# Kernel tuning notes

Hardware: AMD Instinct MI355X
Metric: run time of the kernel (lower is better)

## Reference

```python
import jax, jax.numpy as jnp
import numpy as np

B, S, D, H = 4, 2048, 1024, 16
DK = D // H

def setup_inputs() -> dict:
    key = jax.random.key(0)
    ks = jax.random.split(key, 5)
    scale = D ** -0.5  # keep activations well-scaled for random weights
    return {
        "x": jax.random.normal(ks[0], (B, S, D), dtype=jnp.float32),
        "w_q": jax.random.normal(ks[1], (D, D), dtype=jnp.float32) * scale,
        "w_k": jax.random.normal(ks[2], (D, D), dtype=jnp.float32) * scale,
        "w_v": jax.random.normal(ks[3], (D, D), dtype=jnp.float32) * scale,
        "w_o": jax.random.normal(ks[4], (D, D), dtype=jnp.float32) * scale,
        "b_o": jnp.zeros((D,), dtype=jnp.float32),
    }

def reference(x, w_q, w_k, w_v, w_o, b_o):
    b, s, d = x.shape
    # nn.Linear applies x @ W^T; project then split heads -> [b, h, s, dk]
    q = (x @ w_q.T).reshape(b, s, H, DK).transpose(0, 2, 1, 3)
    k = (x @ w_k.T).reshape(b, s, H, DK).transpose(0, 2, 1, 3)
    v = (x @ w_v.T).reshape(b, s, H, DK).transpose(0, 2, 1, 3)
    scores = jnp.einsum('bhqd,bhkd->bhqk', q, k) * (DK ** -0.5)
    causal = jnp.tril(jnp.ones((s, s), dtype=bool))  # [s, s]
    scores = jnp.where(causal, scores, jnp.float32(-1e9))
    attn = jax.nn.softmax(scores, axis=-1)
    out = jnp.einsum('bhqk,bhkd->bhqd', attn, v)
    out = out.transpose(0, 2, 1, 3).reshape(b, s, d)
    return out @ w_o.T + b_o
```

## Files before the change

kernel.cpp:

```cpp
#include <hip/hip_runtime.h>

typedef unsigned short u16;
typedef unsigned int u32;
typedef __attribute__((ext_vector_type(4))) u16 u16x4;
typedef __attribute__((ext_vector_type(8))) short short8;
typedef __attribute__((ext_vector_type(4))) float f32x4;
typedef __attribute__((ext_vector_type(16))) float f32x16;
typedef __attribute__((ext_vector_type(4))) u32 uint4v;

#define AS1 __attribute__((address_space(1)))
#define AS3 __attribute__((address_space(3)))

#define B_  4
#define S_  2048
#define D_  1024
#define H_  16
#define DK_ 64

#define WAIT_VM(n) asm volatile("s_waitcnt vmcnt(" #n ")" ::: "memory")
#define WAIT_LGK0  asm volatile("s_waitcnt lgkmcnt(0)" ::: "memory")

__device__ __forceinline__ u16 f2bf(float f) {
  union { float f; unsigned u; } v; v.f = f;
  unsigned r = v.u + 0x7fffu + ((v.u >> 16) & 1u);
  return (u16)(r >> 16);
}

__device__ __forceinline__ u32 cvt_pk_bf16(float lo, float hi) {
  u32 r;
  asm("v_cvt_pk_bf16_f32 %0, %1, %2" : "=v"(r) : "v"(lo), "v"(hi));
  return r;
}

__device__ __forceinline__ void pl32_swap(u32& a, u32& b) {
  asm("v_permlane32_swap_b32 %0, %1" : "+v"(a), "+v"(b));
}

__device__ __forceinline__ void gload_lds16(const void* g, void* l) {
  __builtin_amdgcn_global_load_lds((const AS1 void*)g, (AS3 void*)l, 16, 0, 0);
}

__global__ __launch_bounds__(256) void conv_bf16(const float* __restrict__ in,
                                                 u16* __restrict__ out,
                                                 int n, float scale) {
  int i = (blockIdx.x * 256 + threadIdx.x) * 8;
  if (i >= n) return;
  f32x4 a = *reinterpret_cast<const f32x4*>(in + i);
  f32x4 b = *reinterpret_cast<const f32x4*>(in + i + 4);
  union { u16 u[8]; uint4v v; } r;
#pragma unroll
  for (int j = 0; j < 4; ++j) {
    r.u[j]     = f2bf(a[j] * scale);
    r.u[4 + j] = f2bf(b[j] * scale);
  }
  *reinterpret_cast<uint4v*>(out + i) = r.v;
}

__global__ __launch_bounds__(256) void conv_w4(const float* __restrict__ w0,
                                               const float* __restrict__ w1,
                                               const float* __restrict__ w2,
                                               const float* __restrict__ w3,
                                               u16* __restrict__ out, float s0) {
  int y = blockIdx.y;
  const float* src = (y == 0) ? w0 : (y == 1) ? w1 : (y == 2) ? w2 : w3;
  float scale = (y == 0) ? s0 : 1.0f;
  int i = (blockIdx.x * 256 + threadIdx.x) * 8;
  f32x4 a = *reinterpret_cast<const f32x4*>(src + i);
  f32x4 b = *reinterpret_cast<const f32x4*>(src + i + 4);
  union { u16 u[8]; uint4v v; } r;
#pragma unroll
  for (int j = 0; j < 4; ++j) {
    r.u[j]     = f2bf(a[j] * scale);
    r.u[4 + j] = f2bf(b[j] * scale);
  }
  *reinterpret_cast<uint4v*>(out + (size_t)y * (D_ * D_) + i) = r.v;
}

template<int MODE>
__global__ __launch_bounds__(256) void gemm_bt(const u16* __restrict__ A,
                                               const u16* __restrict__ B,
                                               u16* __restrict__ Qb,
                                               u16* __restrict__ Kb,
                                               u16* __restrict__ Vt,
                                               float* __restrict__ Cf,
                                               const float* __restrict__ bias,
                                               int M, int N, int K) {
  __shared__ __attribute__((aligned(16))) u16 As[128 * 64];
  __shared__ __attribute__((aligned(16))) u16 Bs[128 * 64];

  const int t = threadIdx.x;
  const int l = t & 63;
  const int w = t >> 6;
  const int wr = w >> 1, wc = w & 1;
  const int m0 = blockIdx.y * 128;
  const int n0 = blockIdx.x * 128;

  f32x4 zero = {0.f, 0.f, 0.f, 0.f};
  f32x4 acc[4][4];
#pragma unroll
  for (int i = 0; i < 4; ++i)
#pragma unroll
    for (int j = 0; j < 4; ++j) acc[i][j] = zero;

  for (int k0 = 0; k0 < K; k0 += 64) {
    __syncthreads();
#pragma unroll
    for (int i = 0; i < 4; ++i) {
      int slot = i * 256 + t;
      int r = slot >> 3, c = slot & 7;
      const u16* srcA = A + (size_t)(m0 + r) * K + k0 + ((c ^ (r & 7)) * 8);
      gload_lds16(srcA, (char*)As + (size_t)(i * 256 + w * 64) * 16);
      const u16* srcB = B + (size_t)(n0 + r) * K + k0 + ((c ^ (r & 7)) * 8);
      gload_lds16(srcB, (char*)Bs + (size_t)(i * 256 + w * 64) * 16);
    }
    __syncthreads();

#pragma unroll
    for (int kc = 0; kc < 2; ++kc) {
      short8 a[4], bf[4];
      int lc = kc * 4 + (l >> 4);
#pragma unroll
      for (int i = 0; i < 4; ++i) {
        int ra = wr * 64 + i * 16 + (l & 15);
        a[i] = *reinterpret_cast<const short8*>(&As[ra * 64 + ((lc ^ (ra & 7)) * 8)]);
        int rb = wc * 64 + i * 16 + (l & 15);
        bf[i] = *reinterpret_cast<const short8*>(&Bs[rb * 64 + ((lc ^ (rb & 7)) * 8)]);
      }
#pragma unroll
      for (int mi = 0; mi < 4; ++mi)
#pragma unroll
        for (int ni = 0; ni < 4; ++ni)
          acc[mi][ni] = __builtin_amdgcn_mfma_f32_16x16x32_bf16(a[mi], bf[ni], acc[mi][ni], 0, 0, 0);
    }
  }

#pragma unroll
  for (int ni = 0; ni < 4; ++ni) {
    int col = n0 + wc * 64 + ni * 16 + (l & 15);
    float bv = (MODE == 1) ? bias[col] : 0.f;
#pragma unroll
    for (int mi = 0; mi < 4; ++mi) {
      int row0 = m0 + wr * 64 + mi * 16 + (l >> 4) * 4;
      if (MODE == 1) {
#pragma unroll
        for (int r = 0; r < 4; ++r)
          Cf[(size_t)(row0 + r) * N + col] = acc[mi][ni][r] + bv;
      } else {
        if (col < 2048) {
          u16* dst = (col < 1024) ? Qb : Kb;
          int c = col & 1023;
#pragma unroll
          for (int r = 0; r < 4; ++r)
            dst[(size_t)(row0 + r) * 1024 + c] = f2bf(acc[mi][ni][r]);
        } else {
          int vc = col - 2048;
          int bh = (row0 >> 11) * 16 + (vc >> 6);
          int s0 = row0 & 2047;
          u16x4 pk;
#pragma unroll
          for (int r = 0; r < 4; ++r) pk[r] = f2bf(acc[mi][ni][r]);
          *reinterpret_cast<u16x4*>(Vt + ((size_t)(bh * 64 + (vc & 63))) * 2048 + s0) = pk;
        }
      }
    }
  }
}

__global__ __launch_bounds__(256) void attn_fwd(const u16* __restrict__ Q,
                                                const u16* __restrict__ K,
                                                const u16* __restrict__ Vtg,
                                                u16* __restrict__ AO) {
  __shared__ __attribute__((aligned(16))) u16 smem[24576];
  u16* Ksb = smem;
  u16* Vsb = smem + 12288;

  const int t = threadIdx.x;
  const int l = t & 63;
  const int w = t >> 6;
  const int hi = l >> 5;
  const int hi8 = hi * 8, hi4 = hi * 4;
  const int bh = blockIdx.x;
  const int s = 15 - blockIdx.y;
  const size_t qkbase = (size_t)((bh >> 4) * S_) * D_ + (bh & 15) * DK_;
  const u16* Vg = Vtg + (size_t)bh * 64 * S_;

  const int qw = s * 128 + w * 32;
  const int qi = qw + (l & 31);

  short8 qf[4];
#pragma unroll
  for (int c = 0; c < 4; ++c)
    qf[c] = *reinterpret_cast<const short8*>(Q + qkbase + (size_t)qi * D_ + c * 16 + hi8);

  f32x16 o0 = {0,0,0,0,0,0,0,0,0,0,0,0,0,0,0,0};
  f32x16 o1 = {0,0,0,0,0,0,0,0,0,0,0,0,0,0,0,0};
  float m_r = -INFINITY, l_r = 0.f;

  const int nst = 2 * (s + 1);

  auto stage = [&](int jt, u16* kdst, u16* vdst) {
    const u16* Ksrc = K + qkbase + (size_t)(jt * 64) * D_;
    const u16* Vsrc = Vg + jt * 64;
#pragma unroll
    for (int i = 0; i < 2; ++i) {
      int slot = i * 256 + t;
      int r = slot >> 3, c = t & 7;
      gload_lds16(Ksrc + (size_t)r * D_ + ((c ^ (r & 7)) * 8),
                  (char*)kdst + (size_t)(i * 256 + w * 64) * 16);
      gload_lds16(Vsrc + (size_t)r * S_ + ((c ^ (r & 7)) * 8),
                  (char*)vdst + (size_t)(i * 256 + w * 64) * 16);
    }
  };

  stage(0, Ksb, Vsb);
  stage(1, Ksb + 4096, Vsb + 4096);
  stage(2, Ksb + 8192, Vsb + 8192);
  int o0b = 0, o1b = 4096, o2b = 8192;

  for (int it = 0; it < nst; ++it) {
    if (it < nst - 2)       { WAIT_VM(8); }
    else if (it == nst - 2) { WAIT_VM(4); }
    else                    { WAIT_VM(0); }
    __builtin_amdgcn_s_barrier();
    __builtin_amdgcn_sched_barrier(0);

    const int j0 = it * 64;
    u16* ks = Ksb + o0b;
    u16* vs = Vsb + o0b;

    if (j0 <= qw + 31) {
      f32x16 s0 = {0,0,0,0,0,0,0,0,0,0,0,0,0,0,0,0};
      f32x16 s1 = {0,0,0,0,0,0,0,0,0,0,0,0,0,0,0,0};
#pragma unroll
      for (int c = 0; c < 4; ++c) {
        int cl = 2 * c + hi;
        int k0r = l & 31, k1r = (l & 31) + 32;
        short8 kf0 = *reinterpret_cast<const short8*>(&ks[k0r * 64 + ((cl ^ (k0r & 7)) * 8)]);
        short8 kf1 = *reinterpret_cast<const short8*>(&ks[k1r * 64 + ((cl ^ (k1r & 7)) * 8)]);
        s0 = __builtin_amdgcn_mfma_f32_32x32x16_bf16(kf0, qf[c], s0, 0, 0, 0);
        s1 = __builtin_amdgcn_mfma_f32_32x32x16_bf16(kf1, qf[c], s1, 0, 0, 0);
      }
      if (j0 + 63 > qw) {
#pragma unroll
        for (int r = 0; r < 16; ++r) {
          int key = j0 + (r & 3) + 8 * (r >> 2) + hi4;
          if (key > qi) s0[r] = -INFINITY;
          if (key + 32 > qi) s1[r] = -INFINITY;
        }
      }
      {
        float mx = s0[0];
#pragma unroll
        for (int r = 1; r < 16; ++r) mx = fmaxf(mx, s0[r]);
#pragma unroll
        for (int r = 0; r < 16; ++r) mx = fmaxf(mx, s1[r]);
        mx = fmaxf(mx, __shfl_xor(mx, 32));
        if (!__all(mx <= m_r + 11.0f)) {
          float mnew = fmaxf(m_r, mx);
          float rr = exp2f(m_r - mnew);
          m_r = mnew;
          l_r *= rr;
#pragma unroll
          for (int r = 0; r < 16; ++r) { o0[r] *= rr; o1[r] *= rr; }
        }
        float sum = 0.f;
#pragma unroll
        for (int r = 0; r < 16; ++r) { s0[r] = exp2f(s0[r] - m_r); sum += s0[r]; }
#pragma unroll
        for (int r = 0; r < 16; ++r) { s1[r] = exp2f(s1[r] - m_r); sum += s1[r]; }
        sum += __shfl_xor(sum, 32);
        l_r += sum;
      }
#pragma unroll
      for (int ksl = 0; ksl < 4; ++ksl) {
        const int b = 8 * (ksl & 1);
        const f32x16& ps = (ksl < 2) ? s0 : s1;
        u32 c0 = cvt_pk_bf16(ps[b + 0], ps[b + 1]);
        u32 c1 = cvt_pk_bf16(ps[b + 2], ps[b + 3]);
        u32 c2 = cvt_pk_bf16(ps[b + 4], ps[b + 5]);
        u32 c3 = cvt_pk_bf16(ps[b + 6], ps[b + 7]);
        pl32_swap(c0, c2);
        pl32_swap(c1, c3);
        union { u32 u[4]; short8 s; } pa;
        pa.u[0] = c0; pa.u[1] = c1; pa.u[2] = c2; pa.u[3] = c3;
        int cl = 2 * ksl + hi;
        int d0r = l & 31, d1r = (l & 31) + 32;
        short8 vf0 = *reinterpret_cast<const short8*>(&vs[d0r * 64 + ((cl ^ (d0r & 7)) * 8)]);
        short8 vf1 = *reinterpret_cast<const short8*>(&vs[d1r * 64 + ((cl ^ (d1r & 7)) * 8)]);
        o0 = __builtin_amdgcn_mfma_f32_32x32x16_bf16(vf0, pa.s, o0, 0, 0, 0);
        o1 = __builtin_amdgcn_mfma_f32_32x32x16_bf16(vf1, pa.s, o1, 0, 0, 0);
      }
    }

    WAIT_LGK0;
    __builtin_amdgcn_sched_barrier(0);
    __builtin_amdgcn_s_barrier();
    if (it + 3 < nst) stage(it + 3, Ksb + o0b, Vsb + o0b);
    int tmp = o0b; o0b = o1b; o1b = o2b; o2b = tmp;
  }

  float inv = 1.0f / l_r;
  u16* Ob = smem + w * 2304;
#pragma unroll
  for (int acc = 0; acc < 2; ++acc) {
    const f32x16& oo = acc ? o1 : o0;
#pragma unroll
    for (int rp = 0; rp < 8; ++rp) {
      u32 pk = cvt_pk_bf16(oo[2 * rp] * inv, oo[2 * rp + 1] * inv);
      int d0 = ((2 * rp) & 3) + 8 * (rp >> 1) + hi4 + 32 * acc;
      *reinterpret_cast<u32*>(&Ob[(l & 31) * 72 + d0]) = pk;
    }
  }
  __syncthreads();
  int qq = l >> 1;
  int chb = (l & 1) * 4;
#pragma unroll
  for (int c2 = 0; c2 < 4; ++c2) {
    uint4v vv = *reinterpret_cast<const uint4v*>(&Ob[qq * 72 + (chb + c2) * 8]);
    *reinterpret_cast<uint4v*>(&AO[qkbase + (size_t)(qw - w * 32 + w * 32 + qq) * D_ + (chb + c2) * 8]) = vv;
  }
}

extern "C" void kernel_launch(void* const* d_in, const int* in_sizes, int n_in,
                              void* d_out, int out_size, void* d_ws, size_t ws_size,
                              hipStream_t stream) {
  const float* x  = (const float*)d_in[0];
  const float* wq = (const float*)d_in[1];
  const float* wk = (const float*)d_in[2];
  const float* wv = (const float*)d_in[3];
  const float* wo = (const float*)d_in[4];
  const float* bo = (const float*)d_in[5];
  float* out = (float*)d_out;

  char* ws = (char*)d_ws;
  u16* XB   = (u16*)(ws);
  u16* WQKV = (u16*)(ws + (size_t)(16 << 20));
  u16* WOB  = (u16*)(ws + (size_t)(22 << 20));
  u16* Qb   = (u16*)(ws + (size_t)(24 << 20));
  u16* Kb   = (u16*)(ws + (size_t)(40 << 20));
  u16* Vt   = (u16*)(ws + (size_t)(56 << 20));
  u16* AO   = (u16*)(ws + (size_t)(72 << 20));

  const int nx = B_ * S_ * D_;
  const int nw = D_ * D_;

  conv_bf16<<<nx / 2048, 256, 0, stream>>>(x, XB, nx, 1.0f);
  conv_w4<<<dim3(nw / 2048, 4), 256, 0, stream>>>(wq, wk, wv, wo, WQKV,
                                                  0.18033688011112042f);

  gemm_bt<0><<<dim3(3072 / 128, (B_ * S_) / 128), 256, 0, stream>>>(
      XB, WQKV, Qb, Kb, Vt, nullptr, nullptr, B_ * S_, 3072, D_);

  attn_fwd<<<dim3(B_ * H_, 16), 256, 0, stream>>>(Qb, Kb, Vt, AO);

  gemm_bt<1><<<dim3(D_ / 128, (B_ * S_) / 128), 256, 0, stream>>>(
      AO, WOB, nullptr, nullptr, nullptr, out, bo, B_ * S_, D_, D_);
}
```

Before: 183.0 us.

## Double-buffer GEMM LDS tiles with 512-thread 128x256 blocks and async prefetch

Rewrites the projection GEMM kernel to use 512-thread blocks computing 128x256 tiles, with double-buffered LDS staging so the global-to-LDS loads for tile k+2 run while MFMAs consume tile k. Explicit vmcnt waits, raw barriers, sched_barrier and setprio control the overlap. The goal is to hide global memory latency and reuse A tiles across a wider N. The cost is 96KB of LDS per block, which may limit occupancy, and fewer blocks in the grid for the output projection.

```diff
diff --git a/kernel.cpp b/kernel.cpp
--- a/kernel.cpp
+++ b/kernel.cpp
@@ -77,23 +77,24 @@
 }
 
 template<int MODE>
-__global__ __launch_bounds__(256) void gemm_bt(const u16* __restrict__ A,
-                                               const u16* __restrict__ B,
-                                               u16* __restrict__ Qb,
-                                               u16* __restrict__ Kb,
-                                               u16* __restrict__ Vt,
-                                               float* __restrict__ Cf,
-                                               const float* __restrict__ bias,
-                                               int M, int N, int K) {
-  __shared__ __attribute__((aligned(16))) u16 As[128 * 64];
-  __shared__ __attribute__((aligned(16))) u16 Bs[128 * 64];
+__global__ __launch_bounds__(512, 2) void gemm_bt2(const u16* __restrict__ A,
+                                                   const u16* __restrict__ B,
+                                                   u16* __restrict__ Qb,
+                                                   u16* __restrict__ Kb,
+                                                   u16* __restrict__ Vt,
+                                                   float* __restrict__ Cf,
+                                                   const float* __restrict__ bias,
+                                                   int M, int N, int K) {
+  __shared__ __attribute__((aligned(16))) u16 As[2][128 * 64];
+  __shared__ __attribute__((aligned(16))) u16 Bs[2][256 * 64];
 
   const int t = threadIdx.x;
   const int l = t & 63;
-  const int w = t >> 6;
-  const int wr = w >> 1, wc = w & 1;
+  const int wm = (t >> 6) >> 2;
+  const int wn = (t >> 6) & 3;
   const int m0 = blockIdx.y * 128;
-  const int n0 = blockIdx.x * 128;
+  const int n0 = blockIdx.x * 256;
+  const int NT = K >> 6;
 
   f32x4 zero = {0.f, 0.f, 0.f, 0.f};
   f32x4 acc[4][4];
@@ -102,45 +103,69 @@
 #pragma unroll
     for (int j = 0; j < 4; ++j) acc[i][j] = zero;
 
-  for (int k0 = 0; k0 < K; k0 += 64) {
-    __syncthreads();
+  auto stageA = [&](int kt, int buf) {
+#pragma unroll
+    for (int i = 0; i < 2; ++i) {
+      int slot = i * 512 + t;
+      int r = slot >> 3, c = slot & 7;
+      gload_lds16(A + (size_t)(m0 + r) * K + kt * 64 + ((c ^ (r & 7)) * 8),
+                  (char*)&As[buf][0] + (size_t)slot * 16);
+    }
+  };
+  auto stageB = [&](int kt, int buf) {
 #pragma unroll
     for (int i = 0; i < 4; ++i) {
-      int slot = i * 256 + t;
+      int slot = i * 512 + t;
       int r = slot >> 3, c = slot & 7;
-      const u16* srcA = A + (size_t)(m0 + r) * K + k0 + ((c ^ (r & 7)) * 8);
-      gload_lds16(srcA, (char*)As + (size_t)(i * 256 + w * 64) * 16);
-      const u16* srcB = B + (size_t)(n0 + r) * K + k0 + ((c ^ (r & 7)) * 8);
-      gload_lds16(srcB, (char*)Bs + (size_t)(i * 256 + w * 64) * 16);
-    }
-    __syncthreads();
-
+      gload_lds16(B + (size_t)(n0 + r) * K + kt * 64 + ((c ^ (r & 7)) * 8),
+                  (char*)&Bs[buf][0] + (size_t)slot * 16);
+    }
+  };
+
+  stageA(0, 0); stageB(0, 0);
+  stageA(1, 1); stageB(1, 1);
+
+  for (int kt = 0; kt < NT; ++kt) {
+    const int buf = kt & 1;
+    if (kt < NT - 1) { WAIT_VM(6); } else { WAIT_VM(0); }
+    __builtin_amdgcn_s_barrier();
+    __builtin_amdgcn_sched_barrier(0);
+
+    short8 af[2][4], bfr[2][4];
 #pragma unroll
     for (int kc = 0; kc < 2; ++kc) {
-      short8 a[4], bf[4];
       int lc = kc * 4 + (l >> 4);
 #pragma unroll
       for (int i = 0; i < 4; ++i) {
-        int ra = wr * 64 + i * 16 + (l & 15);
-        a[i] = *reinterpret_cast<const short8*>(&As[ra * 64 + ((lc ^ (ra & 7)) * 8)]);
-        int rb = wc * 64 + i * 16 + (l & 15);
-        bf[i] = *reinterpret_cast<const short8*>(&Bs[rb * 64 + ((lc ^ (rb & 7)) * 8)]);
-      }
+        int ra = wm * 64 + i * 16 + (l & 15);
+        af[kc][i] = *reinterpret_cast<const short8*>(&As[buf][ra * 64 + ((lc ^ (ra & 7)) * 8)]);
+        int rb = wn * 64 + i * 16 + (l & 15);
+        bfr[kc][i] = *reinterpret_cast<const short8*>(&Bs[buf][rb * 64 + ((lc ^ (rb & 7)) * 8)]);
+      }
+    }
+    WAIT_LGK0;
+    __builtin_amdgcn_sched_barrier(0);
+    __builtin_amdgcn_s_setprio(1);
+#pragma unroll
+    for (int kc = 0; kc < 2; ++kc)
 #pragma unroll
       for (int mi = 0; mi < 4; ++mi)
 #pragma unroll
         for (int ni = 0; ni < 4; ++ni)
-          acc[mi][ni] = __builtin_amdgcn_mfma_f32_16x16x32_bf16(a[mi], bf[ni], acc[mi][ni], 0, 0, 0);
-    }
+          acc[mi][ni] = __builtin_amdgcn_mfma_f32_16x16x32_bf16(af[kc][mi], bfr[kc][ni], acc[mi][ni], 0, 0, 0);
+    __builtin_amdgcn_s_setprio(0);
+    __builtin_amdgcn_sched_barrier(0);
+    __builtin_amdgcn_s_barrier();
+    if (kt + 2 < NT) { stageA(kt + 2, buf); stageB(kt + 2, buf); }
   }
 
 #pragma unroll
   for (int ni = 0; ni < 4; ++ni) {
-    int col = n0 + wc * 64 + ni * 16 + (l & 15);
+    int col = n0 + wn * 64 + ni * 16 + (l & 15);
     float bv = (MODE == 1) ? bias[col] : 0.f;
 #pragma unroll
     for (int mi = 0; mi < 4; ++mi) {
-      int row0 = m0 + wr * 64 + mi * 16 + (l >> 4) * 4;
+      int row0 = m0 + wm * 64 + mi * 16 + (l >> 4) * 4;
       if (MODE == 1) {
 #pragma unroll
         for (int r = 0; r < 4; ++r)
@@ -348,11 +373,11 @@
   conv_w4<<<dim3(nw / 2048, 4), 256, 0, stream>>>(wq, wk, wv, wo, WQKV,
                                                   0.18033688011112042f);
 
-  gemm_bt<0><<<dim3(3072 / 128, (B_ * S_) / 128), 256, 0, stream>>>(
+  gemm_bt2<0><<<dim3(3072 / 256, (B_ * S_) / 128), 512, 0, stream>>>(
       XB, WQKV, Qb, Kb, Vt, nullptr, nullptr, B_ * S_, 3072, D_);
 
   attn_fwd<<<dim3(B_ * H_, 16), 256, 0, stream>>>(Qb, Kb, Vt, AO);
 
-  gemm_bt<1><<<dim3(D_ / 128, (B_ * S_) / 128), 256, 0, stream>>>(
+  gemm_bt2<1><<<dim3(1024 / 256, (B_ * S_) / 128), 512, 0, stream>>>(
       AO, WOB, nullptr, nullptr, nullptr, out, bo, B_ * S_, D_, D_);
 }
```

Measured after the change: 190.2 us. +3.9%, slower.
